# Kernel optimization log

Measured on AMD Instinct MI355X. Metric: run time of the kernel, lower is better.

Reference implementation:

```python
import jax, jax.numpy as jnp
import numpy as np

F = 16      # frames
NV = 4096   # visual points per frame
NT = 512    # tactile points per frame
M = 4096    # model points
SCALE = 0.1


def setup_inputs() -> dict:
    key = jax.random.key(0)
    ks = jax.random.split(key, 6)
    return {
        "state": jax.random.normal(ks[0], (6,), dtype=jnp.float32) * 0.1,
        "model_points": jax.random.normal(ks[1], (M, 3), dtype=jnp.float32),
        "visual_points": jax.random.normal(ks[2], (F, NV, 3), dtype=jnp.float32),
        "tactile_points": jax.random.normal(ks[3], (F, NT, 3), dtype=jnp.float32),
        "physics_pred_states": jax.random.normal(ks[4], (F, 12), dtype=jnp.float32) * 0.1,
        "delta_time": jax.random.uniform(ks[5], (F,), dtype=jnp.float32, minval=0.01, maxval=0.05),
    }


def _skew(a):
    z = jnp.zeros((), a.dtype)
    return jnp.array([[z, -a[2], a[1]],
                      [a[2], z, -a[0]],
                      [-a[1], a[0], z]])


def _rot_from_omega(omega, dt):
    # Rodrigues: R = I + sin(theta*dt) S + (1 - cos(theta*dt)) S@S, S = skew(omega/|omega|)
    theta = jnp.linalg.norm(omega)
    ax = omega / jnp.clip(theta, 1e-8)
    S = _skew(ax)
    return jnp.eye(3, dtype=omega.dtype) + jnp.sin(theta * dt) * S + (1.0 - jnp.cos(theta * dt)) * (S @ S)


def _chamfer(pred, gt):
    # rows: pred [N,3], cols: gt [M,3]; row-min of squared distances, then mean
    d = (jnp.sum(pred * pred, axis=1)[:, None]
         + jnp.sum(gt * gt, axis=1)[None, :]
         - 2.0 * pred @ gt.T)
    return jnp.mean(jnp.min(d, axis=1))


def reference(state, model_points, visual_points, tactile_points, physics_pred_states, delta_time):
    t0 = state[:3]
    r0 = _rot_from_omega(state[3:], jnp.float32(1.0))  # Euler2Mat modeled as axis-angle

    def pose_step(carry, x):
        t, r = carry
        v, omega, dt = x
        t = t + v * dt
        r = _rot_from_omega(omega, dt) @ r
        return (t, r), (t, r)

    _, (ts, rs) = jax.lax.scan(
        pose_step, (t0, r0),
        (physics_pred_states[1:, 6:9], physics_pred_states[1:, 9:12], delta_time[1:]))
    ts = jnp.concatenate([t0[None], ts], axis=0)  # [F,3]
    rs = jnp.concatenate([r0[None], rs], axis=0)  # [F,3,3]

    def frame_loss(acc, x):
        t, r, vp, tp = x
        vc = ((vp - t) @ r) / SCALE
        tc = ((tp - t) @ r) / SCALE
        acc = acc + _chamfer(vc, model_points) + 0.1 * _chamfer(tc, model_points)
        return acc, None

    E_cd, _ = jax.lax.scan(frame_loss, jnp.zeros((), jnp.float32),
                           (ts, rs, visual_points, tactile_points))
    return E_cd
```

## Files before the change

### kernel.cpp

```cpp
#include <hip/hip_runtime.h>
#include <math.h>

#define F_    16
#define NV_   4096
#define NT_   512
#define M_    4096
#define PPF_  (NV_ + NT_)
#define NPTS_ (F_ * PPF_)
#define SCALE_INV 10.0f

#define TPB   256
#define PTSB  96
#define NBLK  (NPTS_ / PTSB)
#define NG    32
#define MPG   (M_ / NG)
#define CHM   32
#define NCH   (MPG / CHM)
#define FS    33
#define PPL   12

__device__ inline void rot_from_omega(float ox, float oy, float oz, float dt,
                                      float* R) {
    float theta = sqrtf(ox * ox + oy * oy + oz * oz);
    float inv = 1.0f / fmaxf(theta, 1e-8f);
    float ax = ox * inv, ay = oy * inv, az = oz * inv;
    float s = sinf(theta * dt);
    float c = 1.0f - cosf(theta * dt);
    R[0] = 1.0f - c * (ay * ay + az * az);
    R[1] = -s * az + c * ax * ay;
    R[2] =  s * ay + c * ax * az;
    R[3] =  s * az + c * ax * ay;
    R[4] = 1.0f - c * (ax * ax + az * az);
    R[5] = -s * ax + c * ay * az;
    R[6] = -s * ay + c * ax * az;
    R[7] =  s * ax + c * ay * az;
    R[8] = 1.0f - c * (ax * ax + ay * ay);
}

__global__ __launch_bounds__(TPB, 3) void chamfer_one(
    const float* __restrict__ state, const float* __restrict__ model,
    const float* __restrict__ vis, const float* __restrict__ tac,
    const float* __restrict__ phys, const float* __restrict__ dts,
    float* __restrict__ out) {
    __shared__ float4 featD[2][NG * FS];
    __shared__ float4 spts[8][13];
    __shared__ float  sposes[F_ * 12];
    __shared__ float  sRs[F_ * 9];
    __shared__ float  sdt[F_ * 3];
    __shared__ float  sdm[PTSB][NG + 1];
    __shared__ float  sw[2];

    const int t  = threadIdx.x;
    const int g  = t >> 3;
    const int m0 = t & 7;
    const int pl = t & 7;
    const int f  = (blockIdx.x * PTSB) / PPF_;
    const int lbase = blockIdx.x * PTSB - f * PPF_;

    if (t < F_) {
        float ox, oy, oz, dt;
        if (t == 0) { ox = state[3]; oy = state[4]; oz = state[5]; dt = 1.0f; }
        else        { ox = phys[t * 12 + 9]; oy = phys[t * 12 + 10];
                      oz = phys[t * 12 + 11]; dt = dts[t]; }
        float Rs[9];
        rot_from_omega(ox, oy, oz, dt, Rs);
        for (int j = 0; j < 9; ++j) sRs[t * 9 + j] = Rs[j];
        if (t > 0) {
            sdt[t * 3 + 0] = phys[t * 12 + 6] * dt;
            sdt[t * 3 + 1] = phys[t * 12 + 7] * dt;
            sdt[t * 3 + 2] = phys[t * 12 + 8] * dt;
        }
    }
    if (t == 0) {
        float R[9];
        for (int j = 0; j < 9; ++j) R[j] = sRs[j];
        float tr[3] = {state[0], state[1], state[2]};
        for (int i = 0; i < F_; ++i) {
            if (i > 0) {
                tr[0] += sdt[i * 3 + 0];
                tr[1] += sdt[i * 3 + 1];
                tr[2] += sdt[i * 3 + 2];
                float Rn[9];
                const float* Rsp = sRs + i * 9;
                for (int r = 0; r < 3; ++r)
                    for (int c2 = 0; c2 < 3; ++c2)
                        Rn[r * 3 + c2] = Rsp[r * 3 + 0] * R[0 + c2] +
                                         Rsp[r * 3 + 1] * R[3 + c2] +
                                         Rsp[r * 3 + 2] * R[6 + c2];
                for (int j = 0; j < 9; ++j) R[j] = Rn[j];
            }
            float* o = sposes + i * 12;
            o[0] = tr[0]; o[1] = tr[1]; o[2] = tr[2];
            for (int j = 0; j < 9; ++j) o[3 + j] = R[j] * SCALE_INV;
        }
    }

#pragma unroll
    for (int j2 = 0; j2 < 4; ++j2) {
        int id = g * MPG + m0 + 8 * j2;
        float gx = model[id * 3 + 0], gy = model[id * 3 + 1], gz = model[id * 3 + 2];
        featD[0][g * FS + m0 + 8 * j2] =
            make_float4(-2.0f * gx, -2.0f * gy, -2.0f * gz, gx * gx + gy * gy + gz * gz);
    }
    __syncthreads();

    if (t < PTSB) {
        int loc = lbase + t;
        const float* p = (loc < NV_) ? (vis + ((size_t)f * NV_ + loc) * 3)
                                     : (tac + ((size_t)f * NT_ + (loc - NV_)) * 3);
        float px = p[0], py = p[1], pz = p[2];
        const float* ps = sposes + f * 12;
        float d0 = px - ps[0], d1 = py - ps[1], d2 = pz - ps[2];
        const float* R = ps + 3;
        float x = d0 * R[0] + d1 * R[3] + d2 * R[6];
        float y = d0 * R[1] + d1 * R[4] + d2 * R[7];
        float z = d0 * R[2] + d1 * R[5] + d2 * R[8];
        spts[t / PPL][t % PPL] = make_float4(x, y, z, x * x + y * y + z * z);
    }
    __syncthreads();

    float c0[PPL], c1[PPL], c2[PPL], cn[PPL], dm[PPL];
#pragma unroll
    for (int k = 0; k < PPL; ++k) {
        float4 p = spts[pl][k];
        c0[k] = p.x; c1[k] = p.y; c2[k] = p.z; cn[k] = p.w;
        dm[k] = 3.4e38f;
    }

    for (int c = 0; c < NCH; ++c) {
        float mx[4], my[4], mz[4];
        if (c + 1 < NCH) {
#pragma unroll
            for (int j2 = 0; j2 < 4; ++j2) {
                int id = g * MPG + (c + 1) * CHM + m0 + 8 * j2;
                mx[j2] = model[id * 3 + 0];
                my[j2] = model[id * 3 + 1];
                mz[j2] = model[id * 3 + 2];
            }
        }
        const float4* fb = &featD[c & 1][g * FS];
#pragma unroll 8
        for (int m = 0; m < CHM; m += 2) {
            float4 ga = fb[m];
            float4 gb = fb[m + 1];
#pragma unroll
            for (int k = 0; k < PPL; ++k) {
                float da = fmaf(ga.x, c0[k], fmaf(ga.y, c1[k], fmaf(ga.z, c2[k], ga.w)));
                float db = fmaf(gb.x, c0[k], fmaf(gb.y, c1[k], fmaf(gb.z, c2[k], gb.w)));
                dm[k] = fminf(dm[k], fminf(da, db));
            }
        }
        if (c + 1 < NCH) {
#pragma unroll
            for (int j2 = 0; j2 < 4; ++j2) {
                featD[(c + 1) & 1][g * FS + m0 + 8 * j2] =
                    make_float4(-2.0f * mx[j2], -2.0f * my[j2], -2.0f * mz[j2],
                                mx[j2] * mx[j2] + my[j2] * my[j2] + mz[j2] * mz[j2]);
            }
        }
        __syncthreads();
    }

#pragma unroll
    for (int k = 0; k < PPL; ++k) sdm[pl * PPL + k][g] = dm[k] + cn[k];
    __syncthreads();

    float v = 0.0f;
    if (t < PTSB) {
        const float* row = sdm[t];
        float mn = row[0];
#pragma unroll
        for (int i = 1; i < NG; ++i) mn = fminf(mn, row[i]);
        const int loc = lbase + t;
        const float w = (loc < NV_) ? (1.0f / NV_) : (0.1f / NT_);
        v = mn * w;
    }
    if (t < 128) {
#pragma unroll
        for (int off = 32; off > 0; off >>= 1) v += __shfl_down(v, off);
        if ((t & 63) == 0) sw[t >> 6] = v;
    }
    __syncthreads();
    if (t == 0) atomicAdd(out, sw[0] + sw[1]);
}

extern "C" void kernel_launch(void* const* d_in, const int* in_sizes, int n_in,
                              void* d_out, int out_size, void* d_ws, size_t ws_size,
                              hipStream_t stream) {
    const float* state = (const float*)d_in[0];
    const float* model = (const float*)d_in[1];
    const float* vis   = (const float*)d_in[2];
    const float* tac   = (const float*)d_in[3];
    const float* phys  = (const float*)d_in[4];
    const float* dts   = (const float*)d_in[5];
    float* out = (float*)d_out;
    (void)d_ws; (void)ws_size;

    hipMemsetAsync(out, 0, sizeof(float), stream);
    chamfer_one<<<NBLK, TPB, 0, stream>>>(state, model, vis, tac, phys, dts, out);
}
```

Before: 94.56 us.

## Shrink per-thread point tile and compute poses per thread to raise occupancy

Result: slower. 105.7 us (+11.7%).

```diff
diff --git a/kernel.cpp b/kernel.cpp
--- a/kernel.cpp
+++ b/kernel.cpp
@@ -10,14 +10,14 @@
 #define SCALE_INV 10.0f
 
 #define TPB   256
-#define PTSB  96
+#define PTSB  72
 #define NBLK  (NPTS_ / PTSB)
 #define NG    32
 #define MPG   (M_ / NG)
 #define CHM   32
 #define NCH   (MPG / CHM)
 #define FS    33
-#define PPL   12
+#define PPL   9
 
 __device__ inline void rot_from_omega(float ox, float oy, float oz, float dt,
                                       float* R) {
@@ -37,16 +37,12 @@
     R[8] = 1.0f - c * (ax * ax + ay * ay);
 }
 
-__global__ __launch_bounds__(TPB, 3) void chamfer_one(
+__global__ __launch_bounds__(TPB, 4) void chamfer_one(
     const float* __restrict__ state, const float* __restrict__ model,
     const float* __restrict__ vis, const float* __restrict__ tac,
     const float* __restrict__ phys, const float* __restrict__ dts,
     float* __restrict__ out) {
-    __shared__ float4 featD[2][NG * FS];
-    __shared__ float4 spts[8][13];
-    __shared__ float  sposes[F_ * 12];
-    __shared__ float  sRs[F_ * 9];
-    __shared__ float  sdt[F_ * 3];
+    __shared__ float4 feat[NG * FS];
     __shared__ float  sdm[PTSB][NG + 1];
     __shared__ float  sw[2];
 
@@ -57,75 +53,51 @@
     const int f  = (blockIdx.x * PTSB) / PPF_;
     const int lbase = blockIdx.x * PTSB - f * PPF_;
 
-    if (t < F_) {
-        float ox, oy, oz, dt;
-        if (t == 0) { ox = state[3]; oy = state[4]; oz = state[5]; dt = 1.0f; }
-        else        { ox = phys[t * 12 + 9]; oy = phys[t * 12 + 10];
-                      oz = phys[t * 12 + 11]; dt = dts[t]; }
-        float Rs[9];
-        rot_from_omega(ox, oy, oz, dt, Rs);
-        for (int j = 0; j < 9; ++j) sRs[t * 9 + j] = Rs[j];
-        if (t > 0) {
-            sdt[t * 3 + 0] = phys[t * 12 + 6] * dt;
-            sdt[t * 3 + 1] = phys[t * 12 + 7] * dt;
-            sdt[t * 3 + 2] = phys[t * 12 + 8] * dt;
-        }
-    }
-    if (t == 0) {
-        float R[9];
-        for (int j = 0; j < 9; ++j) R[j] = sRs[j];
-        float tr[3] = {state[0], state[1], state[2]};
-        for (int i = 0; i < F_; ++i) {
-            if (i > 0) {
-                tr[0] += sdt[i * 3 + 0];
-                tr[1] += sdt[i * 3 + 1];
-                tr[2] += sdt[i * 3 + 2];
-                float Rn[9];
-                const float* Rsp = sRs + i * 9;
-                for (int r = 0; r < 3; ++r)
-                    for (int c2 = 0; c2 < 3; ++c2)
-                        Rn[r * 3 + c2] = Rsp[r * 3 + 0] * R[0 + c2] +
-                                         Rsp[r * 3 + 1] * R[3 + c2] +
-                                         Rsp[r * 3 + 2] * R[6 + c2];
-                for (int j = 0; j < 9; ++j) R[j] = Rn[j];
-            }
-            float* o = sposes + i * 12;
-            o[0] = tr[0]; o[1] = tr[1]; o[2] = tr[2];
-            for (int j = 0; j < 9; ++j) o[3 + j] = R[j] * SCALE_INV;
-        }
-    }
-
 #pragma unroll
     for (int j2 = 0; j2 < 4; ++j2) {
         int id = g * MPG + m0 + 8 * j2;
         float gx = model[id * 3 + 0], gy = model[id * 3 + 1], gz = model[id * 3 + 2];
-        featD[0][g * FS + m0 + 8 * j2] =
+        feat[g * FS + m0 + 8 * j2] =
             make_float4(-2.0f * gx, -2.0f * gy, -2.0f * gz, gx * gx + gy * gy + gz * gz);
     }
-    __syncthreads();
 
-    if (t < PTSB) {
-        int loc = lbase + t;
-        const float* p = (loc < NV_) ? (vis + ((size_t)f * NV_ + loc) * 3)
-                                     : (tac + ((size_t)f * NT_ + (loc - NV_)) * 3);
-        float px = p[0], py = p[1], pz = p[2];
-        const float* ps = sposes + f * 12;
-        float d0 = px - ps[0], d1 = py - ps[1], d2 = pz - ps[2];
-        const float* R = ps + 3;
-        float x = d0 * R[0] + d1 * R[3] + d2 * R[6];
-        float y = d0 * R[1] + d1 * R[4] + d2 * R[7];
-        float z = d0 * R[2] + d1 * R[5] + d2 * R[8];
-        spts[t / PPL][t % PPL] = make_float4(x, y, z, x * x + y * y + z * z);
+    float R[9], tr[3];
+    {
+        tr[0] = state[0]; tr[1] = state[1]; tr[2] = state[2];
+        rot_from_omega(state[3], state[4], state[5], 1.0f, R);
+        for (int i = 1; i <= f; ++i) {
+            float dt = dts[i];
+            tr[0] += phys[i * 12 + 6] * dt;
+            tr[1] += phys[i * 12 + 7] * dt;
+            tr[2] += phys[i * 12 + 8] * dt;
+            float Rs[9];
+            rot_from_omega(phys[i * 12 + 9], phys[i * 12 + 10], phys[i * 12 + 11], dt, Rs);
+            float Rn[9];
+            for (int r = 0; r < 3; ++r)
+                for (int c2 = 0; c2 < 3; ++c2)
+                    Rn[r * 3 + c2] = Rs[r * 3 + 0] * R[0 + c2] +
+                                     Rs[r * 3 + 1] * R[3 + c2] +
+                                     Rs[r * 3 + 2] * R[6 + c2];
+            for (int j = 0; j < 9; ++j) R[j] = Rn[j];
+        }
+        for (int j = 0; j < 9; ++j) R[j] *= SCALE_INV;
     }
-    __syncthreads();
 
     float c0[PPL], c1[PPL], c2[PPL], cn[PPL], dm[PPL];
 #pragma unroll
     for (int k = 0; k < PPL; ++k) {
-        float4 p = spts[pl][k];
-        c0[k] = p.x; c1[k] = p.y; c2[k] = p.z; cn[k] = p.w;
+        int loc = lbase + pl * PPL + k;
+        const float* p = (loc < NV_) ? (vis + ((size_t)f * NV_ + loc) * 3)
+                                     : (tac + ((size_t)f * NT_ + (loc - NV_)) * 3);
+        float d0 = p[0] - tr[0], d1 = p[1] - tr[1], d2 = p[2] - tr[2];
+        float x = d0 * R[0] + d1 * R[3] + d2 * R[6];
+        float y = d0 * R[1] + d1 * R[4] + d2 * R[7];
+        float z = d0 * R[2] + d1 * R[5] + d2 * R[8];
+        c0[k] = x; c1[k] = y; c2[k] = z;
+        cn[k] = x * x + y * y + z * z;
         dm[k] = 3.4e38f;
     }
+    __syncthreads();
 
     for (int c = 0; c < NCH; ++c) {
         float mx[4], my[4], mz[4];
@@ -138,8 +110,8 @@
                 mz[j2] = model[id * 3 + 2];
             }
         }
-        const float4* fb = &featD[c & 1][g * FS];
-#pragma unroll 8
+        const float4* fb = &feat[g * FS];
+#pragma unroll 4
         for (int m = 0; m < CHM; m += 2) {
             float4 ga = fb[m];
             float4 gb = fb[m + 1];
@@ -147,18 +119,19 @@
             for (int k = 0; k < PPL; ++k) {
                 float da = fmaf(ga.x, c0[k], fmaf(ga.y, c1[k], fmaf(ga.z, c2[k], ga.w)));
                 float db = fmaf(gb.x, c0[k], fmaf(gb.y, c1[k], fmaf(gb.z, c2[k], gb.w)));
-                dm[k] = fminf(dm[k], fminf(da, db));
+                dm[k] = fminf(fminf(da, db), dm[k]);
             }
         }
+        __syncthreads();
         if (c + 1 < NCH) {
 #pragma unroll
             for (int j2 = 0; j2 < 4; ++j2) {
-                featD[(c + 1) & 1][g * FS + m0 + 8 * j2] =
+                feat[g * FS + m0 + 8 * j2] =
                     make_float4(-2.0f * mx[j2], -2.0f * my[j2], -2.0f * mz[j2],
                                 mx[j2] * mx[j2] + my[j2] * my[j2] + mz[j2] * mz[j2]);
             }
+            __syncthreads();
         }
-        __syncthreads();
     }
 
 #pragma unroll
```
